# Optimization experiments

Hardware: AMD Instinct MI355X
Metric: run time of the kernel (lower is better)

Reference implementation:

```python
import jax, jax.numpy as jnp
import numpy as np

B, N, F, T, K, O = 64, 34, 16, 96, 3, 64
EPS = 1e-8  # torch cosine_similarity eps


def _laplacian(A):
    # get_L_d: normalized graph Laplacian L = I - D^{-1/2} A D^{-1/2}
    n = A.shape[-1]
    d = A.sum(-1)                                   # (..., N) row-sum degrees
    dinv = jnp.where(d > 0, jax.lax.rsqrt(jnp.maximum(d, 1e-12)), 0.0)
    I = jnp.eye(n, dtype=A.dtype)
    return I - dinv[..., :, None] * A * dinv[..., None, :]


def _dynamic_adjacency(gs, position, distance):
    # gs: (B,T,N,F); uses features [1:3] as 2-d wind vector
    v = gs[..., 1:3]                                # (B,T,N,2)
    vn = jnp.linalg.norm(v, axis=-1)                # (B,T,N)
    pn = jnp.linalg.norm(position, axis=-1)         # (N,)
    dots = jnp.einsum('btnc,mc->btnm', v, position)  # (B,T,N,N)
    cos = dots / (jnp.maximum(vn, EPS)[..., None] * jnp.maximum(pn, EPS))
    cos = jnp.maximum(cos, 0.0)                     # cosine_sims[cos<=0]=0
    A = cos * vn[..., None] / distance              # wind_speed / distance
    # F.normalize(p=2, dim=(1,2)): per-sample Frobenius normalization
    frob = jnp.sqrt(jnp.sum(A * A, axis=(-2, -1), keepdims=True))
    return A / jnp.maximum(frob, 1e-12)


def setup_inputs() -> dict:
    key = jax.random.key(0)
    ks = jax.random.split(key, 6)
    x = jax.random.normal(ks[0], (B, N, F, T), jnp.float32)
    st_attention = jax.random.normal(ks[1], (B, K, N, N), jnp.float32)
    position = jax.random.normal(ks[2], (N, 2), jnp.float32)
    distance = jax.random.uniform(ks[3], (N, N), jnp.float32, 1.0, 10.0)
    Theta = jax.random.normal(ks[4], (K, F, O), jnp.float32) * 0.1
    Theta_L = jax.random.normal(ks[5], (K, F, O), jnp.float32) * 0.1
    return {"x": x, "st_attention": st_attention, "position": position,
            "distance": distance, "Theta": Theta, "Theta_L": Theta_L}


def reference(x, st_attention, position, distance, Theta, Theta_L):
    Kk = Theta.shape[0]
    gs = jnp.transpose(x, (0, 3, 1, 2))             # (B,T,N,F) -- vectorize over timesteps
    A = _dynamic_adjacency(gs, position, distance)  # (B,T,N,N)
    L1 = _laplacian(A)
    L2 = _laplacian(jnp.swapaxes(A, -1, -2))
    n = A.shape[-1]
    I = jnp.broadcast_to(jnp.eye(n, dtype=A.dtype), L1.shape)
    cheb1, cheb2 = [I, L1], [I, L2]
    for i in range(2, Kk):
        cheb1.append(2.0 * jnp.matmul(L1, cheb1[-1]) - cheb1[-2])
        cheb2.append(2.0 * jnp.matmul(L2, cheb2[-1]) - cheb2[-2])
    # softmax over dim=1 of (B,N,N) slice -> axis 2 of (B,K,N,N)
    att = jax.nn.softmax(st_attention, axis=2)      # (B,K,N,N)
    out = jnp.zeros(gs.shape[:3] + (Theta.shape[-1],), dtype=x.dtype)  # (B,T,N,O)
    for k in range(Kk):
        a = att[:, k][:, None]                       # (B,1,N,N) broadcast over T
        Tk1 = cheb1[k] * a
        Tk2 = cheb2[k] * a
        # T_k_with_att^T @ graph_signal @ theta
        out = out + jnp.einsum('btij,btif,fo->btjo', Tk1, gs, Theta[k]) \
                  + jnp.einsum('btij,btif,fo->btjo', Tk2, gs, Theta_L[k])
    out = jax.nn.relu(out)
    return jnp.transpose(out, (0, 2, 3, 1))          # (B,N,O,T)
```

## Files before the change

### kernel.cpp

```cpp
#include <hip/hip_runtime.h>
#include <cstddef>

namespace {
constexpr int cB = 64, cN = 34, cF = 16, cT = 96, cK = 3, cO = 64;
constexpr int LP = 72;
constexpr int BHP = 88;
constexpr int T4 = cT / 4;
constexpr float cEPS = 1e-8f;
constexpr size_t WS_ATT = 1u << 20;
constexpr size_t H_DW = (size_t)cB * T4 * 136 * 40;

typedef __attribute__((ext_vector_type(8))) _Float16 f16x8;
typedef __attribute__((ext_vector_type(8))) short   s16x8;
typedef __attribute__((ext_vector_type(4))) float   f32x4;

__device__ inline unsigned short f2h(float v) {
    _Float16 h = (_Float16)v;
    return __builtin_bit_cast(unsigned short, h);
}
__device__ inline float h2f(unsigned short u) {
    return (float)__builtin_bit_cast(_Float16, u);
}

template <bool LIN>
__device__ inline size_t hidx(int b, int t4, int j, int tt, int c) {
    if (LIN) return ((size_t)(b * T4 + t4) * 136 + 4 * j + tt) * 40 + c;
    int s = tt * 40 + c;
    return (((size_t)b * cN + j) * cO + (s >> 2)) * cT + 4 * t4 + (s & 3);
}
}

__global__ __launch_bounds__(256) void att_softmax_k(const float* __restrict__ st,
                                                     float* __restrict__ att) {
    int idx = blockIdx.x * blockDim.x + threadIdx.x;
    if (idx >= cB * cK * cN) return;
    int j = idx % cN;
    int bk = idx / cN;
    const float* base = st + (size_t)bk * cN * cN + j;
    float v[cN];
    float m = -3.402823466e38f;
#pragma unroll
    for (int i = 0; i < cN; ++i) { v[i] = base[(size_t)i * cN]; m = fmaxf(m, v[i]); }
    float s = 0.f;
#pragma unroll
    for (int i = 0; i < cN; ++i) { v[i] = __expf(v[i] - m); s += v[i]; }
    float inv = 1.f / s;
    float* ob = att + (size_t)bk * cN * cN + j;
#pragma unroll
    for (int i = 0; i < cN; ++i) ob[(size_t)i * cN] = v[i] * inv;
}

template <bool LIN>
__global__ __launch_bounds__(256, 6) void cheb_h_k(
    const float* __restrict__ x,
    const float* __restrict__ att,
    const float* __restrict__ pos,
    const float* __restrict__ dist,
    unsigned* __restrict__ Hst)
{
    __shared__ __align__(16) unsigned short s_L1[cN * LP];
    __shared__ __align__(16) unsigned short s_L2[cN * LP];
    __shared__ __align__(16) unsigned short s_M1T[cN * LP];
    __shared__ __align__(16) unsigned short s_M3T[cN * LP];
    __shared__ __align__(16) unsigned short s_gsT[cF * LP];
    __shared__ float s_d0[cN], s_v1[cN], s_v2[cN], s_p1[cN], s_p2[cN], s_di1[cN], s_di2[cN];

    const int tid = threadIdx.x;
    const int lane = tid & 63;
    const int w = tid >> 6;
    const int lr = lane & 15;
    const int lg = lane >> 4;
    const int kb8 = lg * 8;

    const unsigned g = blockIdx.x;
    const unsigned lin = (g & 7u) * (cB * cT / 8) + (g >> 3);
    const int b = lin / cT, t = lin % cT;
    const int t4 = t >> 2, tt = t & 3;

    const float* att1 = att + ((size_t)b * cK + 1) * cN * cN;
    const float* att2 = att + ((size_t)b * cK + 2) * cN * cN;

    float distr[5], a1r[5];
#pragma unroll
    for (int e = 0; e < 5; ++e) {
        int idx = tid + 256 * e;
        if (idx < cN * cN) {
            distr[e] = dist[idx];
            a1r[e] = att1[idx];
        }
    }

    {
        f32x4 z = (f32x4){0.f, 0.f, 0.f, 0.f};
        for (int i2 = tid; i2 < cN * LP / 8; i2 += 256) {
            ((f32x4*)s_L1)[i2] = z; ((f32x4*)s_L2)[i2] = z;
            ((f32x4*)s_M1T)[i2] = z; ((f32x4*)s_M3T)[i2] = z;
        }
    }
    if (tid < cN) {
        float px = pos[2 * tid], py = pos[2 * tid + 1];
        float pn = sqrtf(px * px + py * py);
        float r = 1.f / fmaxf(pn, cEPS);
        s_p1[tid] = px * r; s_p2[tid] = py * r;
        s_d0[tid] = att[((size_t)b * cK) * cN * cN + tid * cN + tid];
    } else if (tid >= 64 && tid < 64 + cN) {
        int n = tid - 64;
        float x1 = x[(((size_t)b * cN + n) * cF + 1) * cT + t];
        float x2 = x[(((size_t)b * cN + n) * cF + 2) * cT + t];
        float vn = sqrtf(x1 * x1 + x2 * x2);
        float s = vn / fmaxf(vn, cEPS);
        s_v1[n] = x1 * s; s_v2[n] = x2 * s;
    }
    for (int idx = tid; idx < cF * LP; idx += 256) {
        int f = idx / LP, n = idx - f * LP;
        unsigned short v = 0;
        if (n < cN) v = f2h(x[(((size_t)b * cN + n) * cF + f) * cT + t]);
        s_gsT[idx] = v;
    }
    __syncthreads();

    float* Af = (float*)s_L1;
#pragma unroll
    for (int e = 0; e < 5; ++e) {
        int idx = tid + 256 * e;
        if (idx < cN * cN) {
            int i = idx / cN, m = idx - i * cN;
            float dot = s_v1[i] * s_p1[m] + s_v2[i] * s_p2[m];
            Af[idx] = __fdividef(fmaxf(dot, 0.f), distr[e]);
        }
    }
    __syncthreads();

    if (tid < 136) {
        int s = tid >> 1, half = tid & 1;
        float acc = 0.f;
        if (s < cN) {
            const float* row = Af + s * cN + half * 17;
#pragma unroll
            for (int m = 0; m < 17; ++m) acc += row[m];
        } else {
            int j = s - cN;
            const float* col = Af + half * 17 * cN + j;
#pragma unroll
            for (int i = 0; i < 17; ++i) acc += col[i * cN];
        }
        float tot = acc + __shfl_xor(acc, 1, 64);
        if (half == 0) {
            float d = (tot > 0.f) ? rsqrtf(fmaxf(tot, 1e-12f)) : 0.f;
            if (s < cN) s_di1[s] = d; else s_di2[s - cN] = d;
        }
    }
    float aij[5], aji[5];
#pragma unroll
    for (int e = 0; e < 5; ++e) {
        int idx = tid + 256 * e;
        if (idx < cN * cN) {
            int i = idx / cN, j = idx - i * cN;
            aij[e] = Af[idx];
            aji[e] = Af[j * cN + i];
        }
    }
    __syncthreads();

#pragma unroll
    for (int e = 0; e < 5; ++e) {
        int idx = tid + 256 * e;
        if (idx < cN * cN) {
            int i = idx / cN, j = idx - i * cN;
            float diag = (i == j) ? 1.f : 0.f;
            float l1 = diag - s_di1[i] * aij[e] * s_di1[j];
            float l2 = diag - s_di2[i] * aji[e] * s_di2[j];
            int rm = i * LP + j, tm = j * LP + i;
            s_L1[rm] = f2h(l1);
            s_L1[rm + cN] = 0;
            if (j < 4) s_L1[i * LP + 68 + j] = 0;
            s_L2[rm] = f2h(l2);
            float a1 = a1r[e];
            s_M1T[tm] = f2h(a1 * l1);
            s_M3T[tm] = f2h(a1 * l2);
        }
    }
    __syncthreads();

    const int nnt = (w & 1) ? 1 : 2;
    const int ntb0 = (w & 1) ? 32 : 0;
    float a2r[2][3][2][2];
#pragma unroll
    for (int un = 0; un < 2; ++un) {
        if (un == 1 && nnt < 2) break;
        int jb = ntb0 + un * 16 + lr;
        if (jb < cN) {
#pragma unroll
            for (int mt = 0; mt < 3; ++mt) {
#pragma unroll
                for (int h = 0; h < 2; ++h) {
                    int ia = mt * 16 + lg * 4 + 2 * h;
                    if (ia < cN) {
                        a2r[un][mt][h][0] = att2[ia * cN + jb];
                        a2r[un][mt][h][1] = att2[(ia + 1) * cN + jb];
                    }
                }
            }
        }
    }

    const unsigned short* Ah = (w < 2) ? s_L1 : s_L2;
    f32x4 cd0[3], cd1[3];
#pragma unroll
    for (int mt = 0; mt < 3; ++mt) {
        cd0[mt] = (f32x4){0.f, 0.f, 0.f, 0.f};
        cd1[mt] = (f32x4){0.f, 0.f, 0.f, 0.f};
    }
#pragma unroll
    for (int ks = 0; ks < 2; ++ks) {
        f16x8 fah[3];
#pragma unroll
        for (int mt = 0; mt < 3; ++mt)
            fah[mt] = *(const f16x8*)&Ah[(mt * 16 + lr) * LP + 32 * ks + kb8];
#pragma unroll
        for (int un = 0; un < 2; ++un) {
            if (un == 1 && nnt < 2) break;
            int col = ntb0 + un * 16 + lr;
            s16x8 fbb;
#pragma unroll
            for (int e2 = 0; e2 < 8; ++e2) {
                int kk = 32 * ks + kb8 + e2;
                fbb[e2] = (kk < cN) ? (short)Ah[kk * LP + col] : (short)0;
            }
            f16x8 fb = __builtin_bit_cast(f16x8, fbb);
#pragma unroll
            for (int mt = 0; mt < 3; ++mt) {
                f32x4 acc = un ? cd1[mt] : cd0[mt];
                acc = __builtin_amdgcn_mfma_f32_16x16x32_f16(fah[mt], fb, acc, 0, 0, 0);
                if (un) cd1[mt] = acc; else cd0[mt] = acc;
            }
        }
    }
    __syncthreads();

    {
        unsigned short* Md = (w < 2) ? s_L1 : s_L2;
#pragma unroll
        for (int un = 0; un < 2; ++un) {
            if (un == 1 && nnt < 2) break;
            int jb = ntb0 + un * 16 + lr;
            if (jb < cN) {
#pragma unroll
                for (int mt = 0; mt < 3; ++mt) {
#pragma unroll
                    for (int h = 0; h < 2; ++h) {
                        int ia = mt * 16 + lg * 4 + 2 * h;
                        if (ia < cN) {
                            float dva = h ? (un ? cd1[mt][2] : cd0[mt][2])
                                          : (un ? cd1[mt][0] : cd0[mt][0]);
                            float dvb = h ? (un ? cd1[mt][3] : cd0[mt][3])
                                          : (un ? cd1[mt][1] : cd0[mt][1]);
                            float cva = 2.f * dva - ((ia == jb) ? 1.f : 0.f);
                            float cvb = 2.f * dvb - ((ia + 1 == jb) ? 1.f : 0.f);
                            unsigned lo = f2h(a2r[un][mt][h][0] * cva);
                            unsigned hi = f2h(a2r[un][mt][h][1] * cvb);
                            ((unsigned*)Md)[(jb * LP + ia) >> 1] = lo | (hi << 16);
                        }
                    }
                }
            }
        }
    }
    __syncthreads();

    {
        const unsigned short* Ap = (w == 0) ? s_M1T : (w == 1) ? s_L1
                                 : (w == 2) ? s_M3T : s_L2;
        f32x4 hd[3];
#pragma unroll
        for (int mt = 0; mt < 3; ++mt) hd[mt] = (f32x4){0.f, 0.f, 0.f, 0.f};
#pragma unroll
        for (int ks = 0; ks < 2; ++ks) {
            f16x8 fb = *(const f16x8*)&s_gsT[lr * LP + 32 * ks + kb8];
#pragma unroll
            for (int mt = 0; mt < 3; ++mt) {
                f16x8 fa = *(const f16x8*)&Ap[(mt * 16 + lr) * LP + 32 * ks + kb8];
                hd[mt] = __builtin_amdgcn_mfma_f32_16x16x32_f16(fa, fb, hd[mt], 0, 0, 0);
            }
        }
        for (int idx = tid; idx < cN * 8; idx += 256) {
            int j = idx >> 3, c = idx & 7;
            float d = s_d0[j];
            unsigned lo = f2h(d * h2f(s_gsT[(2 * c) * LP + j]));
            unsigned hi = f2h(d * h2f(s_gsT[(2 * c + 1) * LP + j]));
            Hst[hidx<LIN>(b, t4, j, tt, c)] = lo | (hi << 16);
        }
        const int pc = 16 * (w + 1);
        const int cdw = (pc >> 1) + (lr >> 1);
#pragma unroll
        for (int mt = 0; mt < 3; ++mt) {
#pragma unroll
            for (int r = 0; r < 4; ++r) {
                int j = mt * 16 + lg * 4 + r;
                unsigned mine = (unsigned)f2h(hd[mt][r]);
                unsigned other = __shfl_xor(mine, 1, 64);
                unsigned dword = (lr & 1) ? ((other & 0xffffu) | (mine << 16))
                                          : (mine | (other << 16));
                bool mystore = ((lr & 1) == 0) ? (r < 2) : (r >= 2);
                if (mystore && j < cN)
                    Hst[hidx<LIN>(b, t4, j, tt, cdw)] = dword;
            }
        }
    }
}

template <bool LIN>
__global__ __launch_bounds__(256, 4) void proj_k(
    const unsigned* __restrict__ Hst,
    const float* __restrict__ Th,
    const float* __restrict__ ThL,
    float* __restrict__ out)
{
    __shared__ __align__(16) unsigned short s_H[144 * BHP + 16];

    const int tid = threadIdx.x;
    const int lane = tid & 63;
    const int w = tid >> 6;
    const int lr = lane & 15;
    const int lg = lane >> 4;
    const int kb8 = lg * 8;
    const int ocol = w * 16 + lr;

    const unsigned g = blockIdx.x;
    const unsigned lin = (g & 7u) * (cB * T4 / 8) + (g >> 3);
    const int b = lin / T4, t4 = lin % T4;
    const int t0 = t4 * 4;

    f16x8 bfr[3];
#pragma unroll
    for (int s = 0; s < 3; ++s) {
#pragma unroll
        for (int j = 0; j < 8; ++j) {
            int cc = 32 * s + kb8 + j;
            float v = 0.f;
            if (cc < 80) {
                int p = cc >> 4, f = cc & 15;
                if (p == 0)      v = Th[f * cO + ocol] + ThL[f * cO + ocol];
                else if (p == 1) v = Th[(cF + f) * cO + ocol];
                else if (p == 2) v = Th[(2 * cF + f) * cO + ocol];
                else if (p == 3) v = ThL[(cF + f) * cO + ocol];
                else             v = ThL[(2 * cF + f) * cO + ocol];
            }
            bfr[s][j] = (_Float16)v;
        }
    }

    {
        unsigned* dst = (unsigned*)s_H;
        for (int i2 = tid; i2 < 144 * (BHP / 2); i2 += 256) {
            int r = i2 / (BHP / 2), c = i2 - r * (BHP / 2);
            unsigned v = 0u;
            if (r < 136 && c < 40) {
                v = Hst[hidx<LIN>(b, t4, r >> 2, r & 3, c)];
            }
            dst[i2] = v;
        }
    }
    __syncthreads();

    f32x4 acc[9];
#pragma unroll
    for (int mt = 0; mt < 9; ++mt) acc[mt] = (f32x4){0.f, 0.f, 0.f, 0.f};
#pragma unroll
    for (int s = 0; s < 3; ++s) {
#pragma unroll
        for (int mt = 0; mt < 9; ++mt) {
            f16x8 a = *(const f16x8*)&s_H[(mt * 16 + lr) * BHP + kb8 + 32 * s];
            acc[mt] = __builtin_amdgcn_mfma_f32_16x16x32_f16(a, bfr[s], acc[mt], 0, 0, 0);
        }
    }

#pragma unroll
    for (int mt = 0; mt < 9; ++mt) {
        int j = 4 * mt + lg;
        if (j < cN) {
            float4 v;
            v.x = fmaxf(acc[mt][0], 0.f);
            v.y = fmaxf(acc[mt][1], 0.f);
            v.z = fmaxf(acc[mt][2], 0.f);
            v.w = fmaxf(acc[mt][3], 0.f);
            *(float4*)&out[(((size_t)b * cN + j) * cO + ocol) * cT + t0] = v;
        }
    }
}

extern "C" void kernel_launch(void* const* d_in, const int* in_sizes, int n_in,
                              void* d_out, int out_size, void* d_ws, size_t ws_size,
                              hipStream_t stream) {
    const float* x    = (const float*)d_in[0];
    const float* st   = (const float*)d_in[1];
    const float* pos  = (const float*)d_in[2];
    const float* dist = (const float*)d_in[3];
    const float* Th   = (const float*)d_in[4];
    const float* ThL  = (const float*)d_in[5];
    float* out = (float*)d_out;
    float* att = (float*)d_ws;

    att_softmax_k<<<(cB * cK * cN + 255) / 256, 256, 0, stream>>>(st, att);

    const bool use_ws = ws_size >= WS_ATT + H_DW * 4;
    if (use_ws) {
        unsigned* Hws = (unsigned*)((char*)d_ws + WS_ATT);
        cheb_h_k<true><<<cB * cT, 256, 0, stream>>>(x, att, pos, dist, Hws);
        proj_k<true><<<cB * T4, 256, 0, stream>>>(Hws, Th, ThL, out);
    } else {
        unsigned* Hst = (unsigned*)d_out;
        cheb_h_k<false><<<cB * cT, 256, 0, stream>>>(x, att, pos, dist, Hst);
        proj_k<false><<<cB * T4, 256, 0, stream>>>(Hst, Th, ThL, out);
    }
}
```

Measured before the change: 97.24 us.

## Swizzle transposed LDS tiles and stage H in output buffer only

Result: slower. 101.4 us (+4.3%).

```diff
diff --git a/kernel.cpp b/kernel.cpp
--- a/kernel.cpp
+++ b/kernel.cpp
@@ -7,8 +7,6 @@
 constexpr int BHP = 88;
 constexpr int T4 = cT / 4;
 constexpr float cEPS = 1e-8f;
-constexpr size_t WS_ATT = 1u << 20;
-constexpr size_t H_DW = (size_t)cB * T4 * 136 * 40;
 
 typedef __attribute__((ext_vector_type(8))) _Float16 f16x8;
 typedef __attribute__((ext_vector_type(8))) short   s16x8;
@@ -22,9 +20,7 @@
     return (float)__builtin_bit_cast(_Float16, u);
 }
 
-template <bool LIN>
 __device__ inline size_t hidx(int b, int t4, int j, int tt, int c) {
-    if (LIN) return ((size_t)(b * T4 + t4) * 136 + 4 * j + tt) * 40 + c;
     int s = tt * 40 + c;
     return (((size_t)b * cN + j) * cO + (s >> 2)) * cT + 4 * t4 + (s & 3);
 }
@@ -50,8 +46,7 @@
     for (int i = 0; i < cN; ++i) ob[(size_t)i * cN] = v[i] * inv;
 }
 
-template <bool LIN>
-__global__ __launch_bounds__(256, 6) void cheb_h_k(
+__global__ __launch_bounds__(256, 7) void cheb_h_k(
     const float* __restrict__ x,
     const float* __restrict__ att,
     const float* __restrict__ pos,
@@ -170,14 +165,16 @@
             float diag = (i == j) ? 1.f : 0.f;
             float l1 = diag - s_di1[i] * aij[e] * s_di1[j];
             float l2 = diag - s_di2[i] * aji[e] * s_di2[j];
-            int rm = i * LP + j, tm = j * LP + i;
+            int rm = i * LP + j;
             s_L1[rm] = f2h(l1);
             s_L1[rm + cN] = 0;
             if (j < 4) s_L1[i * LP + 68 + j] = 0;
             s_L2[rm] = f2h(l2);
+            int kj = (j ^ (j >> 3)) & 7;
+            int tmS = j * LP + ((((i >> 3) ^ kj) << 3) | (i & 7));
             float a1 = a1r[e];
-            s_M1T[tm] = f2h(a1 * l1);
-            s_M3T[tm] = f2h(a1 * l2);
+            s_M1T[tmS] = f2h(a1 * l1);
+            s_M3T[tmS] = f2h(a1 * l2);
         }
     }
     __syncthreads();
@@ -271,6 +268,7 @@
     {
         const unsigned short* Ap = (w == 0) ? s_M1T : (w == 1) ? s_L1
                                  : (w == 2) ? s_M3T : s_L2;
+        const bool swz = (w == 0) || (w == 2);
         f32x4 hd[3];
 #pragma unroll
         for (int mt = 0; mt < 3; ++mt) hd[mt] = (f32x4){0.f, 0.f, 0.f, 0.f};
@@ -279,7 +277,10 @@
             f16x8 fb = *(const f16x8*)&s_gsT[lr * LP + 32 * ks + kb8];
 #pragma unroll
             for (int mt = 0; mt < 3; ++mt) {
-                f16x8 fa = *(const f16x8*)&Ap[(mt * 16 + lr) * LP + 32 * ks + kb8];
+                int row = mt * 16 + lr;
+                int blk = 4 * ks + lg;
+                int off = swz ? ((blk ^ ((row ^ (row >> 3)) & 7)) << 3) : (blk << 3);
+                f16x8 fa = *(const f16x8*)&Ap[row * LP + off];
                 hd[mt] = __builtin_amdgcn_mfma_f32_16x16x32_f16(fa, fb, hd[mt], 0, 0, 0);
             }
         }
@@ -288,7 +289,7 @@
             float d = s_d0[j];
             unsigned lo = f2h(d * h2f(s_gsT[(2 * c) * LP + j]));
             unsigned hi = f2h(d * h2f(s_gsT[(2 * c + 1) * LP + j]));
-            Hst[hidx<LIN>(b, t4, j, tt, c)] = lo | (hi << 16);
+            Hst[hidx(b, t4, j, tt, c)] = lo | (hi << 16);
         }
         const int pc = 16 * (w + 1);
         const int cdw = (pc >> 1) + (lr >> 1);
@@ -303,13 +304,12 @@
                                           : (mine | (other << 16));
                 bool mystore = ((lr & 1) == 0) ? (r < 2) : (r >= 2);
                 if (mystore && j < cN)
-                    Hst[hidx<LIN>(b, t4, j, tt, cdw)] = dword;
-            }
-        }
-    }
-}
-
-template <bool LIN>
+                    Hst[hidx(b, t4, j, tt, cdw)] = dword;
+            }
+        }
+    }
+}
+
 __global__ __launch_bounds__(256, 4) void proj_k(
     const unsigned* __restrict__ Hst,
     const float* __restrict__ Th,
@@ -356,7 +356,7 @@
             int r = i2 / (BHP / 2), c = i2 - r * (BHP / 2);
             unsigned v = 0u;
             if (r < 136 && c < 40) {
-                v = Hst[hidx<LIN>(b, t4, r >> 2, r & 3, c)];
+                v = Hst[hidx(b, t4, r >> 2, r & 3, c)];
             }
             dst[i2] = v;
         }
@@ -400,17 +400,9 @@
     const float* ThL  = (const float*)d_in[5];
     float* out = (float*)d_out;
     float* att = (float*)d_ws;
+    unsigned* Hst = (unsigned*)d_out;
 
     att_softmax_k<<<(cB * cK * cN + 255) / 256, 256, 0, stream>>>(st, att);
-
-    const bool use_ws = ws_size >= WS_ATT + H_DW * 4;
-    if (use_ws) {
-        unsigned* Hws = (unsigned*)((char*)d_ws + WS_ATT);
-        cheb_h_k<true><<<cB * cT, 256, 0, stream>>>(x, att, pos, dist, Hws);
-        proj_k<true><<<cB * T4, 256, 0, stream>>>(Hws, Th, ThL, out);
-    } else {
-        unsigned* Hst = (unsigned*)d_out;
-        cheb_h_k<false><<<cB * cT, 256, 0, stream>>>(x, att, pos, dist, Hst);
-        proj_k<false><<<cB * T4, 256, 0, stream>>>(Hst, Th, ThL, out);
-    }
-}
+    cheb_h_k<<<cB * cT, 256, 0, stream>>>(x, att, pos, dist, Hst);
+    proj_k<<<cB * T4, 256, 0, stream>>>(Hst, Th, ThL, out);
+}
```
